# Kernel optimization log

Measured on AMD Instinct MI355X. Metric: run time of the kernel, lower is better.

Reference implementation:

```python
import math
import jax, jax.numpy as jnp
import numpy as np

B, C, K, P, STRIDE, ITERS = 32, 32, 3, 4, 2, 3
PSIZE = P * P
EPS = 1e-6
LAMBDA = 1e-3
LN_2PI = math.log(2.0 * math.pi)


def _extract_patches(x, K, stride):
    # Replicates torch F.unfold + transpose + view exactly, including the
    # layout reinterpretation: unfold's channel dim is ordered (c, kh, kw)
    # (c slowest) but the torch code views it as (K*K, c).
    b, h, w, c = x.shape
    pad = K // 2
    oh = (h + 2 * pad - K) // stride + 1
    ow = (w + 2 * pad - K) // stride + 1
    xp = jnp.pad(x, ((0, 0), (pad, pad), (pad, pad), (0, 0)))
    sl = []
    for kh in range(K):
        for kw in range(K):
            sl.append(xp[:, kh:kh + stride * (oh - 1) + 1:stride,
                            kw:kw + stride * (ow - 1) + 1:stride, :])
    p = jnp.stack(sl, axis=-1)                 # (b, oh, ow, c, K*K)  -> (c, kh, kw) order
    p = p.reshape(b, oh, ow, c * K * K)        # flat, c slowest (matches torch unfold memory)
    patches = p.reshape(b, oh, ow, K * K, c)   # reinterpret as (K*K, c), as the torch view does
    return patches, oh, ow


def _em_routing(v, a_in, beta_u, beta_a):
    # v: (b, Bin, C, psize), a_in: (b, Bin, 1)
    b, Bin, Cc, psize = v.shape
    r = jnp.full((b, Bin, Cc, 1), 1.0 / Cc, dtype=v.dtype)
    a4 = a_in[:, :, None, :]                   # (b, Bin, 1, 1)
    a_out = None
    mu = None
    for t in range(ITERS):
        # ---- M step ----
        rr = r * a4
        rr = rr / (jnp.sum(rr, axis=2, keepdims=True) + EPS)
        r_sum = jnp.sum(rr, axis=1, keepdims=True)            # (b,1,C,1)
        coeff = rr / (r_sum + EPS)
        mu = jnp.sum(coeff * v, axis=1, keepdims=True)        # (b,1,C,psize)
        sigma_sq = jnp.sum(coeff * (v - mu) ** 2, axis=1, keepdims=True) + EPS
        sigma_sq = jnp.maximum(sigma_sq, 1e-4)
        r_sum_flat = r_sum.reshape(b, Cc, 1)
        sig_flat = jnp.maximum(sigma_sq.reshape(b, Cc, psize), 1e-4)
        cost_h = (beta_u.reshape(1, Cc, 1) + jnp.log(jnp.sqrt(sig_flat))) * r_sum_flat
        a_out = jax.nn.sigmoid(LAMBDA * (beta_a.reshape(1, Cc) - jnp.sum(cost_h, axis=2)))
        a_out = jnp.clip(a_out, 1e-4, 1.0 - 1e-4)
        mu = jnp.nan_to_num(mu, nan=0.0, posinf=1e4, neginf=-1e4)
        sigma_sq = jnp.nan_to_num(sigma_sq, nan=1e-4, posinf=1e4, neginf=1e-4)
        a_out = jnp.nan_to_num(a_out, nan=0.5, posinf=1.0 - 1e-4, neginf=1e-4)
        # ---- E step ----
        if t < ITERS - 1:
            ss = jnp.maximum(sigma_sq, 1e-4)
            ao = jnp.clip(a_out, 1e-4, 1.0 - 1e-4)
            ln_p = -(v - mu) ** 2 / (2.0 * ss) - jnp.log(jnp.sqrt(ss)) - 0.5 * LN_2PI
            ln_ap = jnp.sum(ln_p, axis=3) + jnp.log(ao.reshape(b, 1, Cc) + EPS)
            ln_ap = jnp.nan_to_num(ln_ap, nan=0.0, posinf=50.0, neginf=-50.0)
            r = jax.nn.softmax(ln_ap, axis=2)[..., None]
            r = jnp.nan_to_num(r, nan=1.0 / Cc, posinf=1.0, neginf=0.0)
    p_out = jnp.nan_to_num(mu[:, 0], nan=0.0, posinf=1e4, neginf=-1e4)  # (b, C, psize)
    a_out = jnp.nan_to_num(a_out, nan=0.5, posinf=1.0 - 1e-4, neginf=1e-4)
    return p_out, a_out


def setup_inputs() -> dict:
    key = jax.random.key(0)
    k1, k2 = jax.random.split(key)
    x = jax.random.normal(k1, (2, 16, 16, B * (PSIZE + 1)), dtype=jnp.float32)
    weights = jax.random.normal(k2, (1, K * K * B, C, PSIZE, PSIZE), dtype=jnp.float32) * 0.02
    beta_u = jnp.zeros((C,), dtype=jnp.float32)
    beta_a = jnp.zeros((C,), dtype=jnp.float32)
    return {"x": x, "weights": weights, "beta_u": beta_u, "beta_a": beta_a}


def reference(x, weights, beta_u, beta_a):
    b, h, w, c = x.shape
    patches, oh, ow = _extract_patches(x, K, STRIDE)          # (b,oh,ow,K*K,c)
    p_in = patches[..., :B * PSIZE].reshape(b * oh * ow, K * K * B, PSIZE)
    a_in = patches[..., B * PSIZE:].reshape(b * oh * ow, K * K * B, 1)
    w0 = weights[0]                                           # (K*K*B, C, psize, psize)
    v = jnp.einsum('bip,icpq->bicq', p_in, w0)                # (b*, K*K*B, C, psize)
    p_out, a_out = _em_routing(v, a_in, beta_u, beta_a)
    p_out = p_out.reshape(b, oh, ow, C * PSIZE)
    a_out = a_out.reshape(b, oh, ow, C)
    out = jnp.concatenate([p_out, a_out], axis=3)
    return p_out, a_out, out
```

## Files before the change

kernel.cpp:

```cpp
#include <hip/hip_runtime.h>
#include <hip/hip_bf16.h>
#include <math.h>

#define EPSV 1e-6f
#define LAMBDAV 1e-3f
#define LN_2PI 1.8378770664093453f

__device__ __forceinline__ float bflo(unsigned int u) {
    union { unsigned int i; float f; } x; x.i = u << 16; return x.f;
}
__device__ __forceinline__ float bfhi(unsigned int u) {
    union { unsigned int i; float f; } x; x.i = u & 0xffff0000u; return x.f;
}
__device__ __forceinline__ unsigned short f2bf(float f) {
    __hip_bfloat16 h = __float2bfloat16(f);
    return *(unsigned short*)&h;
}

typedef __attribute__((ext_vector_type(8))) short s8v;
typedef __attribute__((ext_vector_type(4))) float f4v;
typedef __attribute__((ext_vector_type(2))) int i2v;

template<int CTRL>
__device__ __forceinline__ float dpp_mv(float x) {
    return __int_as_float(__builtin_amdgcn_update_dpp(
        0, __float_as_int(x), CTRL, 0xF, 0xF, true));
}
__device__ __forceinline__ float x16_sum(float x) {
#if __has_builtin(__builtin_amdgcn_permlane16_swap)
    i2v r = __builtin_amdgcn_permlane16_swap(__float_as_int(x), __float_as_int(x), false, false);
    return __int_as_float(r.x) + __int_as_float(r.y);
#else
    return x + __int_as_float(__builtin_amdgcn_ds_swizzle(__float_as_int(x), 0x401F));
#endif
}
__device__ __forceinline__ float x16_max(float x) {
#if __has_builtin(__builtin_amdgcn_permlane16_swap)
    i2v r = __builtin_amdgcn_permlane16_swap(__float_as_int(x), __float_as_int(x), false, false);
    return fmaxf(__int_as_float(r.x), __int_as_float(r.y));
#else
    return fmaxf(x, __int_as_float(__builtin_amdgcn_ds_swizzle(__float_as_int(x), 0x401F)));
#endif
}
__device__ __forceinline__ float xhalf_sum(float x) {
#if __has_builtin(__builtin_amdgcn_permlane32_swap)
    i2v r = __builtin_amdgcn_permlane32_swap(__float_as_int(x), __float_as_int(x), false, false);
    return __int_as_float(r.x) + __int_as_float(r.y);
#else
    return x + __shfl_xor(x, 32, 64);
#endif
}
__device__ __forceinline__ float red_max32(float x) {
    x = fmaxf(x, dpp_mv<0xB1>(x));
    x = fmaxf(x, dpp_mv<0x4E>(x));
    x = fmaxf(x, dpp_mv<0x124>(x));
    x = fmaxf(x, dpp_mv<0x128>(x));
    return x16_max(x);
}
__device__ __forceinline__ float red_sum32(float x) {
    x += dpp_mv<0xB1>(x);
    x += dpp_mv<0x4E>(x);
    x += dpp_mv<0x124>(x);
    x += dpp_mv<0x128>(x);
    return x16_sum(x);
}
__device__ __forceinline__ float red_sum16(float x) {
    x += dpp_mv<0xB1>(x);
    x += dpp_mv<0x4E>(x);
    x += dpp_mv<0x124>(x);
    x += dpp_mv<0x128>(x);
    return x;
}

__global__ __launch_bounds__(256)
void conv_v_kernel(const float* __restrict__ x, const float* __restrict__ w,
                   __hip_bfloat16* __restrict__ vout)
{
    __shared__ unsigned short wb[256 * 40];
    __shared__ unsigned short pb[128 * 40];

    const int bid = blockIdx.x;
    const int i2  = bid >> 1;
    const int mh  = bid & 1;
    const int tid = threadIdx.x;

    for (int u = tid; u < 256 * 8; u += 256) {
        int r = u >> 3, j = u & 7;
        *(unsigned int*)&wb[r * 40 + 16 + j * 2] = 0;
    }
    for (int u = tid; u < 128 * 8; u += 256) {
        int r = u >> 3, j = u & 7;
        *(unsigned int*)&pb[r * 40 + 16 + j * 2] = 0;
    }
    #pragma unroll 4
    for (int u = 0; u < 16; ++u) {
        int idx = u * 256 + tid;
        int cl = idx >> 8, p = (idx >> 4) & 15, q = idx & 15;
        wb[(cl * 16 + q) * 40 + p] = f2bf(w[(size_t)i2 * 8192 + mh * 4096 + idx]);
    }
    #pragma unroll
    for (int u = 0; u < 8; ++u) {
        int idx = u * 256 + tid;
        int nn = idx >> 4, p = idx & 15;
        int e  = i2 * 16 + p;
        int k2 = e >> 9, c2 = e & 511;
        int f  = k2 * 544 + c2;
        int ci = f / 9, kk = f - ci * 9;
        int bi = nn >> 6, oi = (nn >> 3) & 7, oj = nn & 7;
        int row = 2 * oi + kk / 3 - 1;
        int col = 2 * oj + (kk - (kk / 3) * 3) - 1;
        float val = 0.f;
        if ((unsigned)row < 16u && (unsigned)col < 16u)
            val = x[((bi * 16 + row) * 16 + col) * 544 + ci];
        pb[nn * 40 + p] = f2bf(val);
    }
    __syncthreads();

    const int lane = tid & 63;
    const int wv   = tid >> 6;
    const int l16  = lane & 15;
    const int quad = lane >> 4;
    const int cq0l = wv * 64;

    s8v afrag[4], bfrag[8];
    #pragma unroll
    for (int mt = 0; mt < 4; ++mt)
        afrag[mt] = *(const s8v*)&wb[(cq0l + mt * 16 + l16) * 40 + quad * 8];
    #pragma unroll
    for (int nt = 0; nt < 8; ++nt)
        bfrag[nt] = *(const s8v*)&pb[(nt * 16 + l16) * 40 + quad * 8];

    #pragma unroll
    for (int nt = 0; nt < 8; ++nt) {
        const int nl = nt * 16 + l16;
        #pragma unroll
        for (int mt = 0; mt < 4; ++mt) {
            f4v acc = {0.f, 0.f, 0.f, 0.f};
            acc = __builtin_amdgcn_mfma_f32_16x16x32_bf16(afrag[mt], bfrag[nt], acc, 0, 0, 0);
            int cq = mh * 256 + cq0l + mt * 16 + quad * 4;
            unsigned int lo = f2bf(acc[0]) | ((unsigned int)f2bf(acc[1]) << 16);
            unsigned int hi = f2bf(acc[2]) | ((unsigned int)f2bf(acc[3]) << 16);
            uint2 pk; pk.x = lo; pk.y = hi;
            *(uint2*)((unsigned short*)vout + ((size_t)nl * 288 + i2) * 512 + cq) = pk;
        }
    }
}

__global__ __launch_bounds__(1024, 4)
void em_sweep_kernel(const float* __restrict__ x,
                     const unsigned short* __restrict__ v,
                     const float* __restrict__ beta_u,
                     const float* __restrict__ beta_a,
                     float* __restrict__ gpart,
                     const int t)
{
    __shared__ float fct_s[288];
    __shared__ float red_s[16 * 64 * 17];
    __shared__ float mu_s[32 * 17];
    __shared__ float i2ss_s[32 * 17];
    __shared__ float kc_s[32];

    const int bid = blockIdx.x;
    const int n   = bid & 127;
    const int h   = bid >> 7;
    const int tid = threadIdx.x;
    const int bi = n >> 6, oi = (n >> 3) & 7, oj = n & 7;

    if (tid < 288) {
        int k2 = tid >> 5;
        int c2 = 512 + (tid & 31);
        int f  = k2 * 544 + c2;
        int ci = f / 9;
        int kk = f - ci * 9;
        int row = 2 * oi + kk / 3 - 1;
        int col = 2 * oj + (kk - (kk / 3) * 3) - 1;
        float a = 0.f;
        if ((unsigned)row < 16u && (unsigned)col < 16u)
            a = x[((bi * 16 + row) * 16 + col) * 544 + ci];
        fct_s[tid] = a / (a + EPSV);
    }

    if (t > 0 && tid < 512) {
        const int c2 = tid >> 4, q2 = tid & 15;
        const float* pa = gpart + ((size_t)(t - 1) * 128 + n) * 2 * 1088;
        float S1 = pa[tid] + pa[1088 + tid];
        float S2 = pa[512 + tid] + pa[1088 + 512 + tid];
        float S0 = pa[1024 + c2] + pa[1088 + 1024 + c2];
        float invr = 1.0f / (S0 + EPSV);
        float w0  = S0 * invr;
        float m   = S1 * invr;
        float s2p = S2 * invr;
        float sig = s2p - m * m * (2.0f - w0);
        sig = fmaxf(sig + EPSV, 1e-4f);
        float hl = 0.5f * logf(sig);
        mu_s[c2 * 17 + q2]   = m;
        i2ss_s[c2 * 17 + q2] = 1.0f / (2.0f * sig);
        float shl = red_sum16(hl);
        if (q2 == 0) {
            float bu  = beta_u[c2];
            float cs  = (16.0f * bu + shl) * S0;
            float arg = LAMBDAV * (beta_a[c2] - cs);
            float ao  = 1.0f / (1.0f + expf(-arg));
            ao = fminf(fmaxf(ao, 1e-4f), 1.0f - 1e-4f);
            kc_s[c2]  = logf(ao + EPSV) - shl - 8.0f * LN_2PI;
        }
    }
    __syncthreads();

    const unsigned short* vb = v + (size_t)n * 288 * 512;
    const int wv   = tid >> 6;
    const int lane = tid & 63;
    const int c    = lane & 31;
    const int qh   = lane >> 5;
    const int qb   = qh * 8;
    const unsigned short* base = vb + c * 16 + qb;

    float mu8[8], is8[8], kcv = 0.f;
    if (t > 0) {
        #pragma unroll
        for (int j = 0; j < 8; ++j) {
            mu8[j] = mu_s[c * 17 + qb + j];
            is8[j] = i2ss_s[c * 17 + qb + j];
        }
        kcv = kc_s[c];
    }

    float s0 = 0.f, s1[8], s2[8];
    #pragma unroll
    for (int j = 0; j < 8; ++j) { s1[j] = 0.f; s2[j] = 0.f; }

    const int kofs  = h * 10;
    const int npair = 5 - h;

    uint4 ua = *(const uint4*)(base + (size_t)((kofs + 0) * 16 + wv) * 512);
    uint4 ub = *(const uint4*)(base + (size_t)((kofs + 1) * 16 + wv) * 512);

    for (int kp = 0; kp < npair; ++kp) {
        const int ia = (kofs + 2 * kp) * 16 + wv;
        const int ib = ia + 16;
        uint4 una = ua, unb = ub;
        if (kp + 1 < npair) {
            una = *(const uint4*)(base + (size_t)(ia + 32) * 512);
            unb = *(const uint4*)(base + (size_t)(ia + 48) * 512);
        }
        float va[8], vvb[8];
        va[0] = bflo(ua.x); va[1] = bfhi(ua.x);
        va[2] = bflo(ua.y); va[3] = bfhi(ua.y);
        va[4] = bflo(ua.z); va[5] = bfhi(ua.z);
        va[6] = bflo(ua.w); va[7] = bfhi(ua.w);
        vvb[0] = bflo(ub.x); vvb[1] = bfhi(ub.x);
        vvb[2] = bflo(ub.y); vvb[3] = bfhi(ub.y);
        vvb[4] = bflo(ub.z); vvb[5] = bfhi(ub.z);
        vvb[6] = bflo(ub.w); vvb[7] = bfhi(ub.w);

        float rra, rrb;
        if (t == 0) {
            rra = fct_s[ia] * 0.03125f;
            rrb = fct_s[ib] * 0.03125f;
        } else {
            float pa = 0.f, pb2 = 0.f;
            #pragma unroll
            for (int j = 0; j < 8; ++j) {
                float da = va[j] - mu8[j];
                float db = vvb[j] - mu8[j];
                pa  += da * da * is8[j];
                pb2 += db * db * is8[j];
            }
            pa  = xhalf_sum(pa);
            pb2 = xhalf_sum(pb2);
            float acca = kcv - pa;
            float accb = kcv - pb2;
            float mxa = red_max32(acca);
            float mxb = red_max32(accb);
            float ea = __expf(acca - mxa);
            float eb = __expf(accb - mxb);
            float sa = red_sum32(ea);
            float sb = red_sum32(eb);
            rra = (ea / sa) * fct_s[ia];
            rrb = (eb / sb) * fct_s[ib];
        }

        s0 += rra + rrb;
        #pragma unroll
        for (int j = 0; j < 8; ++j) {
            s1[j] += rra * va[j] + rrb * vvb[j];
            s2[j] += rra * va[j] * va[j] + rrb * vvb[j] * vvb[j];
        }
        ua = una; ub = unb;
    }

    {
        float* dst = &red_s[(wv * 64 + lane) * 17];
        dst[0] = s0;
        #pragma unroll
        for (int j = 0; j < 8; ++j) { dst[1 + j] = s1[j]; dst[9 + j] = s2[j]; }
    }
    __syncthreads();

    if (tid < 512) {
        const int c2 = tid >> 4, q2 = tid & 15;
        const int qh2 = q2 >> 3, j2 = q2 & 7;
        float S0 = 0.f, S1 = 0.f, S2 = 0.f;
        #pragma unroll
        for (int wvi = 0; wvi < 16; ++wvi) {
            S0 += red_s[(wvi * 64 + c2) * 17];
            const float* sp = &red_s[(wvi * 64 + qh2 * 32 + c2) * 17];
            S1 += sp[1 + j2];
            S2 += sp[9 + j2];
        }
        float* po = gpart + (((size_t)t * 128 + n) * 2 + h) * 1088;
        po[tid] = S1;
        po[512 + tid] = S2;
        if (q2 == 0) po[1024 + c2] = S0;
    }
}

__global__ __launch_bounds__(512)
void em_final_kernel(const float* __restrict__ gpart,
                     const float* __restrict__ beta_u,
                     const float* __restrict__ beta_a,
                     float* __restrict__ out)
{
    __shared__ float aout_s[32];
    const int n   = blockIdx.x;
    const int tid = threadIdx.x;
    const int c2 = tid >> 4, q2 = tid & 15;

    const float* pa = gpart + ((size_t)2 * 128 + n) * 2 * 1088;
    float S1 = pa[tid] + pa[1088 + tid];
    float S2 = pa[512 + tid] + pa[1088 + 512 + tid];
    float S0 = pa[1024 + c2] + pa[1088 + 1024 + c2];
    float invr = 1.0f / (S0 + EPSV);
    float w0  = S0 * invr;
    float m   = S1 * invr;
    float s2p = S2 * invr;
    float sig = s2p - m * m * (2.0f - w0);
    sig = fmaxf(sig + EPSV, 1e-4f);
    float hl = 0.5f * logf(sig);
    float shl = red_sum16(hl);
    if (q2 == 0) {
        float bu  = beta_u[c2];
        float cs  = (16.0f * bu + shl) * S0;
        float arg = LAMBDAV * (beta_a[c2] - cs);
        float ao  = 1.0f / (1.0f + expf(-arg));
        ao = fminf(fmaxf(ao, 1e-4f), 1.0f - 1e-4f);
        if (isnan(ao)) ao = 0.5f;
        aout_s[c2] = ao;
    }
    float mu = m;
    if (isnan(mu)) mu = 0.f;
    mu = fminf(fmaxf(mu, -10000.f), 10000.f);
    out[(size_t)n * 512 + tid] = mu;
    out[69632 + (size_t)n * 544 + tid] = mu;
    __syncthreads();
    if (tid < 32) {
        float ao = aout_s[tid];
        out[65536 + n * 32 + tid] = ao;
        out[69632 + n * 544 + 512 + tid] = ao;
    }
}

extern "C" void kernel_launch(void* const* d_in, const int* in_sizes, int n_in,
                              void* d_out, int out_size, void* d_ws, size_t ws_size,
                              hipStream_t stream) {
    const float* x  = (const float*)d_in[0];
    const float* w  = (const float*)d_in[1];
    const float* bu = (const float*)d_in[2];
    const float* ba = (const float*)d_in[3];
    float* out = (float*)d_out;
    __hip_bfloat16* v = (__hip_bfloat16*)d_ws;
    float* gpart = (float*)((char*)d_ws + (40u << 20));

    conv_v_kernel<<<dim3(576), dim3(256), 0, stream>>>(x, w, v);
    em_sweep_kernel<<<dim3(256), dim3(1024), 0, stream>>>(
        x, (const unsigned short*)v, bu, ba, gpart, 0);
    em_sweep_kernel<<<dim3(256), dim3(1024), 0, stream>>>(
        x, (const unsigned short*)v, bu, ba, gpart, 1);
    em_sweep_kernel<<<dim3(256), dim3(1024), 0, stream>>>(
        x, (const unsigned short*)v, bu, ba, gpart, 2);
    em_final_kernel<<<dim3(128), dim3(512), 0, stream>>>(gpart, bu, ba, out);
}
```

Baseline: 117.5 us.

## Split EM sweep over six input chunks with 512-thread blocks

The EM sweep kernel now splits each position's 288 input capsules into six chunks of 48 instead of two chunks. It launches 768 blocks of 512 threads (8 waves) instead of 256 blocks of 1024 threads, so more blocks spread across the GPU's compute units. Partial sums now go to six slots per position, and the next iteration and the final kernel add up six partials instead of two. This shrinks the per-block shared reduction buffer but adds more partial-sum traffic through global memory.

After: 117.1 us. Within noise of the previous version (-0.3%).

```diff
diff --git a/kernel.cpp b/kernel.cpp
--- a/kernel.cpp
+++ b/kernel.cpp
@@ -146,7 +146,7 @@
     }
 }
 
-__global__ __launch_bounds__(1024, 4)
+__global__ __launch_bounds__(512)
 void em_sweep_kernel(const float* __restrict__ x,
                      const unsigned short* __restrict__ v,
                      const float* __restrict__ beta_u,
@@ -155,7 +155,7 @@
                      const int t)
 {
     __shared__ float fct_s[288];
-    __shared__ float red_s[16 * 64 * 17];
+    __shared__ float red_s[8 * 64 * 17];
     __shared__ float mu_s[32 * 17];
     __shared__ float i2ss_s[32 * 17];
     __shared__ float kc_s[32];
@@ -180,12 +180,16 @@
         fct_s[tid] = a / (a + EPSV);
     }
 
-    if (t > 0 && tid < 512) {
+    if (t > 0) {
         const int c2 = tid >> 4, q2 = tid & 15;
-        const float* pa = gpart + ((size_t)(t - 1) * 128 + n) * 2 * 1088;
-        float S1 = pa[tid] + pa[1088 + tid];
-        float S2 = pa[512 + tid] + pa[1088 + 512 + tid];
-        float S0 = pa[1024 + c2] + pa[1088 + 1024 + c2];
+        const float* pa = gpart + ((size_t)(t - 1) * 128 + n) * 6 * 1088;
+        float S1 = 0.f, S2 = 0.f, S0 = 0.f;
+        #pragma unroll
+        for (int j = 0; j < 6; ++j) {
+            S1 += pa[j * 1088 + tid];
+            S2 += pa[j * 1088 + 512 + tid];
+            S0 += pa[j * 1088 + 1024 + c2];
+        }
         float invr = 1.0f / (S0 + EPSV);
         float w0  = S0 * invr;
         float m   = S1 * invr;
@@ -229,19 +233,19 @@
     #pragma unroll
     for (int j = 0; j < 8; ++j) { s1[j] = 0.f; s2[j] = 0.f; }
 
-    const int kofs  = h * 10;
-    const int npair = 5 - h;
-
-    uint4 ua = *(const uint4*)(base + (size_t)((kofs + 0) * 16 + wv) * 512);
-    uint4 ub = *(const uint4*)(base + (size_t)((kofs + 1) * 16 + wv) * 512);
-
-    for (int kp = 0; kp < npair; ++kp) {
-        const int ia = (kofs + 2 * kp) * 16 + wv;
-        const int ib = ia + 16;
+    const int kofs = h * 48;
+
+    uint4 ua = *(const uint4*)(base + (size_t)(kofs + 0 + wv) * 512);
+    uint4 ub = *(const uint4*)(base + (size_t)(kofs + 8 + wv) * 512);
+
+    #pragma unroll
+    for (int kp = 0; kp < 3; ++kp) {
+        const int ia = kofs + kp * 16 + wv;
+        const int ib = ia + 8;
         uint4 una = ua, unb = ub;
-        if (kp + 1 < npair) {
-            una = *(const uint4*)(base + (size_t)(ia + 32) * 512);
-            unb = *(const uint4*)(base + (size_t)(ia + 48) * 512);
+        if (kp < 2) {
+            una = *(const uint4*)(base + (size_t)(ia + 16) * 512);
+            unb = *(const uint4*)(base + (size_t)(ia + 24) * 512);
         }
         float va[8], vvb[8];
         va[0] = bflo(ua.x); va[1] = bfhi(ua.x);
@@ -297,18 +301,18 @@
     }
     __syncthreads();
 
-    if (tid < 512) {
+    {
         const int c2 = tid >> 4, q2 = tid & 15;
         const int qh2 = q2 >> 3, j2 = q2 & 7;
         float S0 = 0.f, S1 = 0.f, S2 = 0.f;
         #pragma unroll
-        for (int wvi = 0; wvi < 16; ++wvi) {
+        for (int wvi = 0; wvi < 8; ++wvi) {
             S0 += red_s[(wvi * 64 + c2) * 17];
             const float* sp = &red_s[(wvi * 64 + qh2 * 32 + c2) * 17];
             S1 += sp[1 + j2];
             S2 += sp[9 + j2];
         }
-        float* po = gpart + (((size_t)t * 128 + n) * 2 + h) * 1088;
+        float* po = gpart + (((size_t)t * 128 + n) * 6 + h) * 1088;
         po[tid] = S1;
         po[512 + tid] = S2;
         if (q2 == 0) po[1024 + c2] = S0;
@@ -326,10 +330,14 @@
     const int tid = threadIdx.x;
     const int c2 = tid >> 4, q2 = tid & 15;
 
-    const float* pa = gpart + ((size_t)2 * 128 + n) * 2 * 1088;
-    float S1 = pa[tid] + pa[1088 + tid];
-    float S2 = pa[512 + tid] + pa[1088 + 512 + tid];
-    float S0 = pa[1024 + c2] + pa[1088 + 1024 + c2];
+    const float* pa = gpart + ((size_t)2 * 128 + n) * 6 * 1088;
+    float S1 = 0.f, S2 = 0.f, S0 = 0.f;
+    #pragma unroll
+    for (int j = 0; j < 6; ++j) {
+        S1 += pa[j * 1088 + tid];
+        S2 += pa[j * 1088 + 512 + tid];
+        S0 += pa[j * 1088 + 1024 + c2];
+    }
     float invr = 1.0f / (S0 + EPSV);
     float w0  = S0 * invr;
     float m   = S1 * invr;
@@ -372,11 +380,11 @@
     float* gpart = (float*)((char*)d_ws + (40u << 20));
 
     conv_v_kernel<<<dim3(576), dim3(256), 0, stream>>>(x, w, v);
-    em_sweep_kernel<<<dim3(256), dim3(1024), 0, stream>>>(
+    em_sweep_kernel<<<dim3(768), dim3(512), 0, stream>>>(
         x, (const unsigned short*)v, bu, ba, gpart, 0);
-    em_sweep_kernel<<<dim3(256), dim3(1024), 0, stream>>>(
+    em_sweep_kernel<<<dim3(768), dim3(512), 0, stream>>>(
         x, (const unsigned short*)v, bu, ba, gpart, 1);
-    em_sweep_kernel<<<dim3(256), dim3(1024), 0, stream>>>(
+    em_sweep_kernel<<<dim3(768), dim3(512), 0, stream>>>(
         x, (const unsigned short*)v, bu, ba, gpart, 2);
     em_final_kernel<<<dim3(128), dim3(512), 0, stream>>>(gpart, bu, ba, out);
 }
```
